# Optimization experiments

Hardware: AMD Instinct MI355X
Metric: run time of the kernel (lower is better)

The kernel has to match this reference:

```python
import jax, jax.numpy as jnp
import numpy as np

N = 100000  # nodes


def _gcn_prep(edge_index):
    # PyG GCNConv(normalize=True): add self loops, symmetric deg^{-1/2} norm.
    row = jnp.concatenate([edge_index[0], jnp.arange(N, dtype=edge_index.dtype)])
    col = jnp.concatenate([edge_index[1], jnp.arange(N, dtype=edge_index.dtype)])
    deg = jax.ops.segment_sum(jnp.ones(row.shape[0], dtype=jnp.float32), col, num_segments=N)
    deg_isqrt = jnp.where(deg > 0, jax.lax.rsqrt(jnp.maximum(deg, 1.0)), 0.0)
    norm = deg_isqrt[row] * deg_isqrt[col]  # [E+N]
    return row, col, norm


def _gcn_conv(x, W, b, row, col, norm):
    h = x @ W                                  # [N, out]
    msg = h[row] * norm[:, None]               # [E+N, out] gather + scale
    out = jax.ops.segment_sum(msg, col, num_segments=N)  # scatter-add
    return out + b


def setup_inputs() -> dict:
    key = jax.random.key(0)
    ks = jax.random.split(key, 7)
    E = 3200000
    x = jax.random.normal(ks[0], (N, 100), dtype=jnp.float32)
    edge_index = jax.random.randint(ks[1], (2, E), 0, N, dtype=jnp.int32)
    def glorot(k, fi, fo):
        s = (6.0 / (fi + fo)) ** 0.5
        return jax.random.uniform(k, (fi, fo), jnp.float32, -s, s)
    return {
        "x": x, "edge_index": edge_index,
        "W1": glorot(ks[2], 100, 64), "b1": jnp.zeros((64,), jnp.float32),
        "W2": glorot(ks[3], 64, 64),  "b2": jnp.zeros((64,), jnp.float32),
        "W3": glorot(ks[4], 64, 64),  "b3": jnp.zeros((64,), jnp.float32),
        "Wo": glorot(ks[5], 64, 18),  "bo": jnp.zeros((18,), jnp.float32),
    }


def reference(x, edge_index, W1, b1, W2, b2, W3, b3, Wo, bo):
    row, col, norm = _gcn_prep(edge_index)
    # eval mode: F.dropout(training=False) is identity
    h = jax.nn.relu(_gcn_conv(x, W1, b1, row, col, norm))
    h = jax.nn.relu(_gcn_conv(h, W2, b2, row, col, norm))
    h = jax.nn.relu(_gcn_conv(h, W3, b3, row, col, norm))
    return _gcn_conv(h, Wo, bo, row, col, norm)
```

## Files before the change

kernel.cpp:

```cpp
#include <hip/hip_runtime.h>
#include <hip/hip_fp16.h>

#define NODES 100000
#define NBKT 782
#define HCHUNK 8192
#define FCHUNK 4096

typedef unsigned short u16;
typedef unsigned int u32;

__device__ __forceinline__ float bflo(u32 v) { return __uint_as_float(v << 16); }
__device__ __forceinline__ float bfhi(u32 v) { return __uint_as_float(v & 0xFFFF0000u); }
__device__ __forceinline__ u16 f2bf(float f) {
  u32 x = __float_as_uint(f);
  return (u16)((x + 0x7FFFu + ((x >> 16) & 1u)) >> 16);
}


__global__ __launch_bounds__(256) void zero_k(int* __restrict__ p, int n) {
  int i = blockIdx.x * 256 + threadIdx.x;
  if (i < n) p[i] = 0;
}


__global__ __launch_bounds__(256) void bucket_hist_k(const int* __restrict__ col,
                                                     int* __restrict__ bcnt, int E) {
  __shared__ int h[NBKT];
  int t = threadIdx.x;
  for (int i = t; i < NBKT; i += 256) h[i] = 0;
  __syncthreads();
  int base = blockIdx.x * HCHUNK;
#pragma unroll 4
  for (int j = 0; j < HCHUNK / 256; ++j) {
    int i = base + j * 256 + t;
    if (i < E) atomicAdd(&h[col[i] >> 7], 1);
  }
  __syncthreads();
  for (int i = t; i < NBKT; i += 256) {
    int c = h[i];
    if (c) atomicAdd(&bcnt[i], c);
  }
}

__global__ __launch_bounds__(256) void bscan_k(const int* __restrict__ bcnt,
                                               int* __restrict__ boffs,
                                               int* __restrict__ bcurs, int nb, int E) {
  __shared__ int lds[256];
  int t = threadIdx.x;
  int base = t * 4;
  int v[4];
#pragma unroll
  for (int j = 0; j < 4; ++j) v[j] = (base + j < nb) ? bcnt[base + j] : 0;
  int s = v[0] + v[1] + v[2] + v[3];
  lds[t] = s;
  __syncthreads();
  for (int off = 1; off < 256; off <<= 1) {
    int y = (t >= off) ? lds[t - off] : 0;
    __syncthreads();
    lds[t] += y;
    __syncthreads();
  }
  int excl = lds[t] - s;
#pragma unroll
  for (int j = 0; j < 4; ++j) {
    int i = base + j;
    if (i < nb) { boffs[i] = excl; bcurs[i] = excl; }
    excl += v[j];
  }
  if (t == 255) boffs[nb] = E;
}

__global__ __launch_bounds__(256) void bucket_fill_k(const int* __restrict__ row,
                                                     const int* __restrict__ col,
                                                     int* __restrict__ bcurs,
                                                     u32* __restrict__ recs, int E) {
  __shared__ int lcnt[NBKT];
  __shared__ int lbase[NBKT];
  int t = threadIdx.x;
  int base = blockIdx.x * FCHUNK;
  for (int i = t; i < NBKT; i += 256) lcnt[i] = 0;
  __syncthreads();
  u32 rec[FCHUNK / 256];
  u32 meta[FCHUNK / 256];
#pragma unroll
  for (int j = 0; j < FCHUNK / 256; ++j) {
    int i = base + j * 256 + t;
    if (i < E) {
      int r = row[i], c = col[i];
      int b = c >> 7;
      rec[j] = (u32)r | ((u32)(c & 127) << 17);
      int lr = atomicAdd(&lcnt[b], 1);
      meta[j] = (u32)lr | ((u32)b << 16);
    } else {
      meta[j] = 0xFFFFFFFFu;
    }
  }
  __syncthreads();
  for (int i = t; i < NBKT; i += 256) {
    int c = lcnt[i];
    lbase[i] = c ? atomicAdd(&bcurs[i], c) : 0;
  }
  __syncthreads();
#pragma unroll
  for (int j = 0; j < FCHUNK / 256; ++j) {
    if (meta[j] != 0xFFFFFFFFu) {
      int b = meta[j] >> 16;
      int lr = meta[j] & 0xFFFF;
      recs[lbase[b] + lr] = rec[j];
    }
  }
}

__global__ __launch_bounds__(256) void csr_k(const u32* __restrict__ recs,
                                             const int* __restrict__ boffs,
                                             int* __restrict__ offs, int* __restrict__ adj,
                                             float* __restrict__ dis, int N, int E) {
  __shared__ int cnt[128];
  __shared__ int sa[128], sb[128];
  __shared__ int cur[128];
  int b = blockIdx.x, t = threadIdx.x;
  if (t < 128) cnt[t] = 0;
  __syncthreads();
  int s = boffs[b], e = boffs[b + 1];
  for (int i = s + t; i < e; i += 256) atomicAdd(&cnt[recs[i] >> 17], 1);
  __syncthreads();
  if (t < 128) sa[t] = cnt[t];
  __syncthreads();
#pragma unroll
  for (int off = 1; off < 128; off <<= 1) {
    if (t < 128) sb[t] = sa[t] + ((t >= off) ? sa[t - off] : 0);
    __syncthreads();
    if (t < 128) sa[t] = sb[t];
    __syncthreads();
  }
  if (t < 128) {
    int c = b * 128 + t;
    if (c < N) {
      int excl = sa[t] - cnt[t];
      offs[c] = s + excl;
      cur[t] = s + excl;
      dis[c] = rsqrtf((float)(cnt[t] + 1));
    }
  }
  if (b == 0 && t == 0) offs[N] = E;
  __syncthreads();
  for (int i = s + t; i < e; i += 256) {
    u32 r = recs[i];
    int p = atomicAdd(&cur[r >> 17], 1);
    adj[p] = (int)(r & 0x1FFFF);
  }
}

template <int K, int CHUNK, int NOUT, int OUTFMT>
__global__ __launch_bounds__(256) void gemm_reg_k(const float* __restrict__ X,
                                                  const float* __restrict__ W,
                                                  const float* __restrict__ dis,
                                                  u16* __restrict__ G, int n) {
  static_assert(K % CHUNK == 0 && CHUNK % 4 == 0, "chunking");
  int node = blockIdx.x * 256 + threadIdx.x;
  bool live = node < n;
  int cn = live ? node : 0;
  const float* xrow = X + (size_t)cn * K;
  float acc[NOUT];
#pragma unroll
  for (int j = 0; j < NOUT; ++j) acc[j] = 0.f;
  for (int kc = 0; kc < K; kc += CHUNK) {
    float xv[CHUNK];
#pragma unroll
    for (int q = 0; q < CHUNK / 4; ++q)
      *(float4*)&xv[4 * q] = *(const float4*)(xrow + kc + 4 * q);
#pragma unroll
    for (int kk = 0; kk < CHUNK; ++kk) {
      float a = xv[kk];
      const float* wr = W + (size_t)(kc + kk) * NOUT;
#pragma unroll
      for (int j = 0; j < NOUT; ++j) acc[j] = fmaf(a, wr[j], acc[j]);
    }
  }
  if (!live) return;
  float sc = dis[node];
  if (NOUT == 64) {
    u32 os[32];
#pragma unroll
    for (int j = 0; j < 32; ++j) {
      float v0 = acc[2 * j] * sc, v1 = acc[2 * j + 1] * sc;
      u16 lo = (OUTFMT == 1) ? f2bf(v0) : __half_as_ushort(__float2half(v0));
      u16 hi = (OUTFMT == 1) ? f2bf(v1) : __half_as_ushort(__float2half(v1));
      os[j] = (u32)lo | ((u32)hi << 16);
    }
    uint4* G4 = (uint4*)G;
#pragma unroll
    for (int q = 0; q < 8; ++q)
      G4[(size_t)node * 8 + q] = make_uint4(os[4 * q], os[4 * q + 1], os[4 * q + 2], os[4 * q + 3]);
  } else {
    u32 os[9];
#pragma unroll
    for (int j = 0; j < 9; ++j) {
      float v0 = acc[2 * j] * sc, v1 = acc[2 * j + 1] * sc;
      u16 lo = __half_as_ushort(__float2half(v0));
      u16 hi = __half_as_ushort(__float2half(v1));
      os[j] = (u32)lo | ((u32)hi << 16);
    }
    u32* G32 = (u32*)G;
#pragma unroll
    for (int j = 0; j < 9; ++j) G32[(size_t)node * 9 + j] = os[j];
  }
}

__global__ __launch_bounds__(256) void agg_bf16_k(const u16* __restrict__ g,
                                                  const int* __restrict__ offs,
                                                  const int* __restrict__ adj,
                                                  const float* __restrict__ dis,
                                                  const float* __restrict__ bias,
                                                  float* __restrict__ out, int n) {
  int node = blockIdx.x * 4 + (threadIdx.x >> 6);
  int lane = threadIdx.x & 63;
  int half = lane >> 5, fl = lane & 31;
  if (node >= n) return;
  const u32* g32 = (const u32*)g;
  float acc0 = 0.f, acc1 = 0.f;
  int s = offs[node], e = offs[node + 1];
  int i = s;
  for (; i + 16 <= e; i += 16) {
    int r0 = adj[i + half];
    int r1 = adj[i + 2 + half];
    int r2 = adj[i + 4 + half];
    int r3 = adj[i + 6 + half];
    int r4 = adj[i + 8 + half];
    int r5 = adj[i + 10 + half];
    int r6 = adj[i + 12 + half];
    int r7 = adj[i + 14 + half];
    u32 v0 = g32[(r0 << 5) + fl];
    u32 v1 = g32[(r1 << 5) + fl];
    u32 v2 = g32[(r2 << 5) + fl];
    u32 v3 = g32[(r3 << 5) + fl];
    u32 v4 = g32[(r4 << 5) + fl];
    u32 v5 = g32[(r5 << 5) + fl];
    u32 v6 = g32[(r6 << 5) + fl];
    u32 v7 = g32[(r7 << 5) + fl];
    acc0 += ((bflo(v0) + bflo(v1)) + (bflo(v2) + bflo(v3))) +
            ((bflo(v4) + bflo(v5)) + (bflo(v6) + bflo(v7)));
    acc1 += ((bfhi(v0) + bfhi(v1)) + (bfhi(v2) + bfhi(v3))) +
            ((bfhi(v4) + bfhi(v5)) + (bfhi(v6) + bfhi(v7)));
  }
  for (; i + 8 <= e; i += 8) {
    int r0 = adj[i + half];
    int r1 = adj[i + 2 + half];
    int r2 = adj[i + 4 + half];
    int r3 = adj[i + 6 + half];
    u32 v0 = g32[(r0 << 5) + fl];
    u32 v1 = g32[(r1 << 5) + fl];
    u32 v2 = g32[(r2 << 5) + fl];
    u32 v3 = g32[(r3 << 5) + fl];
    acc0 += (bflo(v0) + bflo(v1)) + (bflo(v2) + bflo(v3));
    acc1 += (bfhi(v0) + bfhi(v1)) + (bfhi(v2) + bfhi(v3));
  }
  for (; i + 2 <= e; i += 2) {
    int r = adj[i + half];
    u32 v = g32[(r << 5) + fl];
    acc0 += bflo(v);
    acc1 += bfhi(v);
  }
  if (i < e) {
    int r = adj[i];
    u32 v = g32[(r << 5) + fl];
    if (half == 0) { acc0 += bflo(v); acc1 += bfhi(v); }
  }
  acc0 += __shfl_xor(acc0, 32, 64);
  acc1 += __shfl_xor(acc1, 32, 64);
  u32 vs = g32[(node << 5) + fl];
  acc0 += bflo(vs);
  acc1 += bfhi(vs);
  float d = dis[node];
  float o0 = fmaxf(fmaf(d, acc0, bias[2 * fl]), 0.f);
  float o1 = fmaxf(fmaf(d, acc1, bias[2 * fl + 1]), 0.f);
  if (half == 0) {
    float2 st = {o0, o1};
    *(float2*)(out + node * 64 + 2 * fl) = st;
  }
}

__global__ __launch_bounds__(256) void agg_f16o_k(const u16* __restrict__ g,
                                                  const int* __restrict__ offs,
                                                  const int* __restrict__ adj,
                                                  const float* __restrict__ dis,
                                                  const float* __restrict__ bias,
                                                  float* __restrict__ out, int n) {
  int node = blockIdx.x * 4 + (threadIdx.x >> 6);
  int lane = threadIdx.x & 63;
  int half = lane >> 5, fl = lane & 31;
  if (node >= n) return;
  const __half* gh = (const __half*)g;
  bool act = fl < 18;
  float acc = 0.f;
  int s = offs[node], e = offs[node + 1];
  int i = s;
  if (act) {
    for (; i + 16 <= e; i += 16) {
      int r0 = adj[i + half];
      int r1 = adj[i + 2 + half];
      int r2 = adj[i + 4 + half];
      int r3 = adj[i + 6 + half];
      int r4 = adj[i + 8 + half];
      int r5 = adj[i + 10 + half];
      int r6 = adj[i + 12 + half];
      int r7 = adj[i + 14 + half];
      float a0 = __half2float(gh[r0 * 18 + fl]);
      float a1 = __half2float(gh[r1 * 18 + fl]);
      float a2 = __half2float(gh[r2 * 18 + fl]);
      float a3 = __half2float(gh[r3 * 18 + fl]);
      float a4 = __half2float(gh[r4 * 18 + fl]);
      float a5 = __half2float(gh[r5 * 18 + fl]);
      float a6 = __half2float(gh[r6 * 18 + fl]);
      float a7 = __half2float(gh[r7 * 18 + fl]);
      acc += ((a0 + a1) + (a2 + a3)) + ((a4 + a5) + (a6 + a7));
    }
    for (; i + 8 <= e; i += 8) {
      int r0 = adj[i + half];
      int r1 = adj[i + 2 + half];
      int r2 = adj[i + 4 + half];
      int r3 = adj[i + 6 + half];
      float a0 = __half2float(gh[r0 * 18 + fl]);
      float a1 = __half2float(gh[r1 * 18 + fl]);
      float a2 = __half2float(gh[r2 * 18 + fl]);
      float a3 = __half2float(gh[r3 * 18 + fl]);
      acc += (a0 + a1) + (a2 + a3);
    }
    for (; i + 2 <= e; i += 2) acc += __half2float(gh[adj[i + half] * 18 + fl]);
    if (i < e && half == 0) acc += __half2float(gh[adj[i] * 18 + fl]);
  }
  acc += __shfl_xor(acc, 32, 64);
  if (act) {
    acc += __half2float(gh[node * 18 + fl]);
    float v = fmaf(dis[node], acc, bias[fl]);
    if (half == 0) out[node * 18 + fl] = v;
  }
}


extern "C" void kernel_launch(void* const* d_in, const int* in_sizes, int n_in,
                              void* d_out, int out_size, void* d_ws, size_t ws_size,
                              hipStream_t stream) {
  const float* x  = (const float*)d_in[0];
  const int*   ei = (const int*)d_in[1];
  const float* W1 = (const float*)d_in[2];
  const float* b1 = (const float*)d_in[3];
  const float* W2 = (const float*)d_in[4];
  const float* b2 = (const float*)d_in[5];
  const float* W3 = (const float*)d_in[6];
  const float* b3 = (const float*)d_in[7];
  const float* Wo = (const float*)d_in[8];
  const float* bo = (const float*)d_in[9];
  float* out = (float*)d_out;

  const int N = NODES;
  const int E = in_sizes[1] / 2;
  const int* rowp = ei;
  const int* colp = ei + E;

  char* p = (char*)d_ws;
  auto alloc = [&](size_t bytes) {
    void* r = (void*)p;
    p += (bytes + 255) & ~(size_t)255;
    return r;
  };
  int*   bcnt  = (int*)alloc((size_t)NBKT * 4);
  int*   bcurs = (int*)alloc((size_t)NBKT * 4);
  int*   boffs = (int*)alloc((size_t)(NBKT + 1) * 4);
  float* dis   = (float*)alloc((size_t)N * 4);
  int*   offs  = (int*)alloc((size_t)(N + 1) * 4);
  int*   adj   = (int*)alloc((size_t)E * 4);
  u32*   recs  = (u32*)alloc((size_t)N * 64 * 2);
  u16*   gb    = (u16*)recs;
  float* h     = (float*)alloc((size_t)N * 64 * 4);
  u16*   g4    = (u16*)alloc((size_t)N * 18 * 2);

  zero_k<<<(NBKT + 255) / 256, 256, 0, stream>>>(bcnt, NBKT);
  bucket_hist_k<<<(E + HCHUNK - 1) / HCHUNK, 256, 0, stream>>>(colp, bcnt, E);
  bscan_k<<<1, 256, 0, stream>>>(bcnt, boffs, bcurs, NBKT, E);
  bucket_fill_k<<<(E + FCHUNK - 1) / FCHUNK, 256, 0, stream>>>(rowp, colp, bcurs, recs, E);
  csr_k<<<NBKT, 256, 0, stream>>>(recs, boffs, offs, adj, dis, N, E);

  int gG = (N + 255) / 256;
  int gA = (N + 3) / 4;

  gemm_reg_k<100, 20, 64, 1><<<gG, 256, 0, stream>>>(x, W1, dis, gb, N);
  agg_bf16_k<<<gA, 256, 0, stream>>>(gb, offs, adj, dis, b1, h, N);

  gemm_reg_k<64, 16, 64, 1><<<gG, 256, 0, stream>>>(h, W2, dis, gb, N);
  agg_bf16_k<<<gA, 256, 0, stream>>>(gb, offs, adj, dis, b2, h, N);

  gemm_reg_k<64, 16, 64, 1><<<gG, 256, 0, stream>>>(h, W3, dis, gb, N);
  agg_bf16_k<<<gA, 256, 0, stream>>>(gb, offs, adj, dis, b3, h, N);

  gemm_reg_k<64, 16, 18, 2><<<gG, 256, 0, stream>>>(h, Wo, dis, g4, N);
  agg_f16o_k<<<gA, 256, 0, stream>>>(g4, offs, adj, dis, bo, out, N);
}
```

Before: 497.2 us.

## Restructure dense GEMMs: LDS-staged weights, 4-thread output split per node pair

Replaces the one-thread-per-node register GEMM with kernels that stage W in shared memory. Each node row is split across a quad of threads (a pair for the 18-wide output). Each thread loads a slice of X and broadcasts it with shuffles, then computes 16 outputs for two nodes. This cuts per-thread register pressure and replaces scalar global W reads with LDS reads, and it also spreads the row loads more evenly across threads. The cost is extra shuffles and LDS traffic, and the grid is doubled.

```diff
diff --git a/kernel.cpp b/kernel.cpp
--- a/kernel.cpp
+++ b/kernel.cpp
@@ -151,59 +151,138 @@
   }
 }
 
-template <int K, int CHUNK, int NOUT, int OUTFMT>
-__global__ __launch_bounds__(256) void gemm_reg_k(const float* __restrict__ X,
-                                                  const float* __restrict__ W,
-                                                  const float* __restrict__ dis,
-                                                  u16* __restrict__ G, int n) {
-  static_assert(K % CHUNK == 0 && CHUNK % 4 == 0, "chunking");
-  int node = blockIdx.x * 256 + threadIdx.x;
-  bool live = node < n;
-  int cn = live ? node : 0;
-  const float* xrow = X + (size_t)cn * K;
-  float acc[NOUT];
-#pragma unroll
-  for (int j = 0; j < NOUT; ++j) acc[j] = 0.f;
-  for (int kc = 0; kc < K; kc += CHUNK) {
-    float xv[CHUNK];
-#pragma unroll
-    for (int q = 0; q < CHUNK / 4; ++q)
-      *(float4*)&xv[4 * q] = *(const float4*)(xrow + kc + 4 * q);
-#pragma unroll
-    for (int kk = 0; kk < CHUNK; ++kk) {
-      float a = xv[kk];
-      const float* wr = W + (size_t)(kc + kk) * NOUT;
-#pragma unroll
-      for (int j = 0; j < NOUT; ++j) acc[j] = fmaf(a, wr[j], acc[j]);
-    }
-  }
-  if (!live) return;
+template <int K, int NK, int OUTFMT>
+__global__ __launch_bounds__(256, 2) void gemm64_k(const float* __restrict__ X,
+                                                   const float* __restrict__ W,
+                                                   const float* __restrict__ dis,
+                                                   u16* __restrict__ G, int n) {
+  static_assert(K == NK * 4, "NT=4");
+  __shared__ float ws[K * 64];
+  int t = threadIdx.x;
+  for (int i = t; i < K * 64; i += 256) ws[i] = W[i];
+  __syncthreads();
+  int q = t & 3, g = t >> 2;
+  int b0 = blockIdx.x * 128;
+  int n0 = b0 + g, n1 = b0 + 64 + g;
+  int c0 = (n0 < n) ? n0 : 0, c1 = (n1 < n) ? n1 : 0;
+  float xv0[NK], xv1[NK];
+  const float* p0 = X + (size_t)c0 * K + q * NK;
+  const float* p1 = X + (size_t)c1 * K + q * NK;
+  if constexpr (NK % 4 == 0) {
+#pragma unroll
+    for (int i = 0; i < NK / 4; ++i) {
+      *(float4*)&xv0[4 * i] = *(const float4*)(p0 + 4 * i);
+      *(float4*)&xv1[4 * i] = *(const float4*)(p1 + 4 * i);
+    }
+  } else {
+#pragma unroll
+    for (int i = 0; i < NK; ++i) { xv0[i] = p0[i]; xv1[i] = p1[i]; }
+  }
+  float acc0[16], acc1[16];
+#pragma unroll
+  for (int j = 0; j < 16; ++j) { acc0[j] = 0.f; acc1[j] = 0.f; }
+  for (int qq = 0; qq < 4; ++qq) {
+    const float* wbase = ws + (size_t)qq * NK * 64 + q * 16;
+#pragma unroll
+    for (int i = 0; i < NK; ++i) {
+      float a0 = __shfl(xv0[i], qq, 4);
+      float a1 = __shfl(xv1[i], qq, 4);
+      const float* wr = wbase + i * 64;
+#pragma unroll
+      for (int j = 0; j < 16; ++j) {
+        float w = wr[j];
+        acc0[j] = fmaf(a0, w, acc0[j]);
+        acc1[j] = fmaf(a1, w, acc1[j]);
+      }
+    }
+  }
+  uint4* G4 = (uint4*)G;
+  {
+    if (n0 < n) {
+      float sc = dis[n0];
+      u32 os[8];
+#pragma unroll
+      for (int j = 0; j < 8; ++j) {
+        float v0 = acc0[2 * j] * sc, v1 = acc0[2 * j + 1] * sc;
+        u16 lo = (OUTFMT == 1) ? f2bf(v0) : __half_as_ushort(__float2half(v0));
+        u16 hi = (OUTFMT == 1) ? f2bf(v1) : __half_as_ushort(__float2half(v1));
+        os[j] = (u32)lo | ((u32)hi << 16);
+      }
+      size_t rb = (size_t)n0 * 8 + q * 2;
+      G4[rb]     = make_uint4(os[0], os[1], os[2], os[3]);
+      G4[rb + 1] = make_uint4(os[4], os[5], os[6], os[7]);
+    }
+    if (n1 < n) {
+      float sc = dis[n1];
+      u32 os[8];
+#pragma unroll
+      for (int j = 0; j < 8; ++j) {
+        float v0 = acc1[2 * j] * sc, v1 = acc1[2 * j + 1] * sc;
+        u16 lo = (OUTFMT == 1) ? f2bf(v0) : __half_as_ushort(__float2half(v0));
+        u16 hi = (OUTFMT == 1) ? f2bf(v1) : __half_as_ushort(__float2half(v1));
+        os[j] = (u32)lo | ((u32)hi << 16);
+      }
+      size_t rb = (size_t)n1 * 8 + q * 2;
+      G4[rb]     = make_uint4(os[0], os[1], os[2], os[3]);
+      G4[rb + 1] = make_uint4(os[4], os[5], os[6], os[7]);
+    }
+  }
+}
+
+__global__ __launch_bounds__(256, 2) void gemm18_k(const float* __restrict__ X,
+                                                   const float* __restrict__ W,
+                                                   const float* __restrict__ dis,
+                                                   u16* __restrict__ G, int n) {
+  __shared__ float ws[64 * 18];
+  int t = threadIdx.x;
+  for (int i = t; i < 64 * 18; i += 256) ws[i] = W[i];
+  __syncthreads();
+  int q = t & 1, g = t >> 1;
+  int b0 = blockIdx.x * 128;
+  int node = b0 + g;
+  int cn = (node < n) ? node : 0;
+  float xv[32];
+  const float* p = X + (size_t)cn * 64 + q * 32;
+#pragma unroll
+  for (int i = 0; i < 8; ++i) *(float4*)&xv[4 * i] = *(const float4*)(p + 4 * i);
+  int cnt = q ? 8 : 10;
+  float acc[10];
+#pragma unroll
+  for (int j = 0; j < 10; ++j) acc[j] = 0.f;
+  for (int qq = 0; qq < 2; ++qq) {
+    const float* wbase = ws + (size_t)qq * 32 * 18 + q * 10;
+#pragma unroll
+    for (int i = 0; i < 32; ++i) {
+      float a = __shfl(xv[i], qq, 2);
+      const float* wr = wbase + i * 18;
+#pragma unroll
+      for (int j = 0; j < 10; ++j)
+        if (j < cnt) acc[j] = fmaf(a, wr[j], acc[j]);
+    }
+  }
+  if (node >= n) return;
   float sc = dis[node];
-  if (NOUT == 64) {
-    u32 os[32];
-#pragma unroll
-    for (int j = 0; j < 32; ++j) {
-      float v0 = acc[2 * j] * sc, v1 = acc[2 * j + 1] * sc;
-      u16 lo = (OUTFMT == 1) ? f2bf(v0) : __half_as_ushort(__float2half(v0));
-      u16 hi = (OUTFMT == 1) ? f2bf(v1) : __half_as_ushort(__float2half(v1));
+  u32* G32 = (u32*)G;
+  if (q == 0) {
+    u32 os[5];
+#pragma unroll
+    for (int j = 0; j < 5; ++j) {
+      u16 lo = __half_as_ushort(__float2half(acc[2 * j] * sc));
+      u16 hi = __half_as_ushort(__float2half(acc[2 * j + 1] * sc));
       os[j] = (u32)lo | ((u32)hi << 16);
     }
-    uint4* G4 = (uint4*)G;
-#pragma unroll
-    for (int q = 0; q < 8; ++q)
-      G4[(size_t)node * 8 + q] = make_uint4(os[4 * q], os[4 * q + 1], os[4 * q + 2], os[4 * q + 3]);
+#pragma unroll
+    for (int j = 0; j < 5; ++j) G32[(size_t)node * 9 + j] = os[j];
   } else {
-    u32 os[9];
-#pragma unroll
-    for (int j = 0; j < 9; ++j) {
-      float v0 = acc[2 * j] * sc, v1 = acc[2 * j + 1] * sc;
-      u16 lo = __half_as_ushort(__float2half(v0));
-      u16 hi = __half_as_ushort(__float2half(v1));
+    u32 os[4];
+#pragma unroll
+    for (int j = 0; j < 4; ++j) {
+      u16 lo = __half_as_ushort(__float2half(acc[2 * j] * sc));
+      u16 hi = __half_as_ushort(__float2half(acc[2 * j + 1] * sc));
       os[j] = (u32)lo | ((u32)hi << 16);
     }
-    u32* G32 = (u32*)G;
-#pragma unroll
-    for (int j = 0; j < 9; ++j) G32[(size_t)node * 9 + j] = os[j];
+#pragma unroll
+    for (int j = 0; j < 4; ++j) G32[(size_t)node * 9 + 5 + j] = os[j];
   }
 }
 
@@ -381,18 +460,18 @@
   bucket_fill_k<<<(E + FCHUNK - 1) / FCHUNK, 256, 0, stream>>>(rowp, colp, bcurs, recs, E);
   csr_k<<<NBKT, 256, 0, stream>>>(recs, boffs, offs, adj, dis, N, E);
 
-  int gG = (N + 255) / 256;
+  int gG = (N + 127) / 128;
   int gA = (N + 3) / 4;
 
-  gemm_reg_k<100, 20, 64, 1><<<gG, 256, 0, stream>>>(x, W1, dis, gb, N);
+  gemm64_k<100, 25, 1><<<gG, 256, 0, stream>>>(x, W1, dis, gb, N);
   agg_bf16_k<<<gA, 256, 0, stream>>>(gb, offs, adj, dis, b1, h, N);
 
-  gemm_reg_k<64, 16, 64, 1><<<gG, 256, 0, stream>>>(h, W2, dis, gb, N);
+  gemm64_k<64, 16, 1><<<gG, 256, 0, stream>>>(h, W2, dis, gb, N);
   agg_bf16_k<<<gA, 256, 0, stream>>>(gb, offs, adj, dis, b2, h, N);
 
-  gemm_reg_k<64, 16, 64, 1><<<gG, 256, 0, stream>>>(h, W3, dis, gb, N);
+  gemm64_k<64, 16, 1><<<gG, 256, 0, stream>>>(h, W3, dis, gb, N);
   agg_bf16_k<<<gA, 256, 0, stream>>>(gb, offs, adj, dis, b3, h, N);
 
-  gemm_reg_k<64, 16, 18, 2><<<gG, 256, 0, stream>>>(h, Wo, dis, g4, N);
+  gemm18_k<<<gG, 256, 0, stream>>>(h, Wo, dis, g4, N);
   agg_f16o_k<<<gA, 256, 0, stream>>>(g4, offs, adj, dis, bo, out, N);
 }
```

Result: faster. 439.5 us (-11.6%).
